# Kernel tuning notes

Measured on AMD Instinct MI355X. Metric: run time of the kernel, lower is better.

Reference implementation:

```python
import jax, jax.numpy as jnp
import numpy as np
import math

B, S, D = 4, 4096, 512

def setup_inputs() -> dict:
    key = jax.random.key(0)
    k_tok, k1, k2, k3 = jax.random.split(key, 4)
    scale = 1.0 / math.sqrt(D)
    return {
        "token": jax.random.normal(k_tok, (B, S, D), dtype=jnp.float32),
        "W1": jax.random.normal(k1, (D, D), dtype=jnp.float32) * scale,
        "W2": jax.random.normal(k2, (D, D), dtype=jnp.float32) * scale,
        "W3": jax.random.normal(k3, (D, D), dtype=jnp.float32) * scale,
    }

def reference(token, W1, W2, W3):
    # nn.Linear(dim, dim, bias=False): y = x @ W.T; W stored as [out, in]
    q = jnp.einsum('bsd,ed->bse', token, W1)  # t1(token)
    k = jnp.einsum('bsd,ed->bse', token, W2)  # t2(token)
    v = jnp.einsum('bsd,ed->bse', token, W3)  # t3(token)
    logits = jnp.einsum('bse,bte->bst', q, k) / jnp.sqrt(jnp.float32(token.shape[-1]))
    scores = jax.nn.softmax(logits, axis=-1)  # full [B,S,S] materialized, as in source
    return jnp.einsum('bst,bte->bse', scores, v)
```

## Files before the change

kernel.cpp:

```cpp
#include <hip/hip_runtime.h>
#include <stdint.h>


#define BDIM 4
#define SDIM 4096
#define DDIM 512
#define MROWS (BDIM * SDIM)
#define XB_ELEMS ((size_t)MROWS * DDIM)
#define W_ELEMS ((size_t)DDIM * DDIM)

typedef short short8_t __attribute__((ext_vector_type(8)));
typedef short short4_t __attribute__((ext_vector_type(4)));
typedef float float4_t __attribute__((ext_vector_type(4)));

typedef __attribute__((address_space(1))) void gvoid_t;
typedef __attribute__((address_space(3))) void lvoid_t;

__device__ __forceinline__ short f2bf(float f) {
    union { float f; uint32_t u; } v; v.f = f;
    uint32_t r = v.u + 0x7FFFu + ((v.u >> 16) & 1u);
    return (short)(r >> 16);
}
__device__ __forceinline__ float bf2f(short s) {
    union { uint32_t u; float f; } v; v.u = ((uint32_t)(uint16_t)s) << 16;
    return v.f;
}

__global__ void detect_kernel(const uint32_t* __restrict__ tok, int* __restrict__ flag) {
    __shared__ int red[256];
    const int tid = threadIdx.x;
    int c = 0;
    for (int i = tid; i < 4096; i += 256) {
        uint32_t e = (tok[i] >> 7) & 0xFFu;
        c += (e >= 105u && e <= 135u) ? 1 : 0;
    }
    red[tid] = c;
    __syncthreads();
    for (int s = 128; s > 0; s >>= 1) {
        if (tid < s) red[tid] += red[tid + s];
        __syncthreads();
    }
    if (tid == 0) *flag = (red[0] > 2048) ? 1 : 0;
}

__global__ void convert_kernel(const void* __restrict__ X, const void* __restrict__ W1,
                               const void* __restrict__ W2, const void* __restrict__ W3,
                               short* __restrict__ dst, const int* __restrict__ flagp,
                               float* __restrict__ RS)
{
    const int bid = blockIdx.x;
    if (bid < 64) RS[bid * 256 + threadIdx.x] = 0.f;
    const int bf16in = *flagp;
    if (bf16in) return;
    const size_t i4 = ((size_t)bid * 256 + threadIdx.x) * 4;
    const void* src; size_t off;
    if (i4 < XB_ELEMS) { src = X; off = i4; }
    else {
        const size_t j = i4 - XB_ELEMS;
        const int g = (int)(j / W_ELEMS);
        src = (g == 0) ? W1 : (g == 1) ? W2 : W3;
        off = j - (size_t)g * W_ELEMS;
    }
    float4 v = *(const float4*)((const float*)src + off);
    short4_t s = { f2bf(v.x), f2bf(v.y), f2bf(v.z), f2bf(v.w) };
    *(short4_t*)(dst + i4) = s;
}

__device__ __forceinline__ void gemm_core(
    const short* __restrict__ A, int lda,
    const short* __restrict__ B, int ldb,
    int m0, int n0, int kIters,
    short* As, short* Bs, float4_t acc[4][4])
{
    const int tid = threadIdx.x;
    const int w = tid >> 6, lane = tid & 63, quad = lane >> 4, l16 = lane & 15;
    const int wm = w >> 1, wn = w & 1;
    const int srow = lane >> 3;
    const int scol = 8 * ((lane & 7) ^ srow);
    const int rsw = l16 & 7;

    for (int kk = 0; kk < kIters; ++kk) {
        const int k0 = 64 * kk;
        __syncthreads();
#pragma unroll
        for (int c = 0; c < 4; ++c) {
            const int rb = 8 * (4 * c + w);
            const short* g = A + (size_t)(m0 + rb + srow) * lda + k0 + scol;
            __builtin_amdgcn_global_load_lds((const gvoid_t*)g,
                (lvoid_t*)(As + rb * 64), 16, 0, 0);
        }
#pragma unroll
        for (int c = 0; c < 4; ++c) {
            const int rb = 8 * (4 * c + w);
            const short* g = B + (size_t)(n0 + rb + srow) * ldb + k0 + scol;
            __builtin_amdgcn_global_load_lds((const gvoid_t*)g,
                (lvoid_t*)(Bs + rb * 64), 16, 0, 0);
        }
        __syncthreads();

#pragma unroll
        for (int k2 = 0; k2 < 2; ++k2) {
            short8_t af[4], bfr[4];
#pragma unroll
            for (int mt = 0; mt < 4; ++mt)
                af[mt] = *(const short8_t*)&As[(64 * wm + 16 * mt + l16) * 64
                                               + 8 * ((quad + 4 * k2) ^ rsw)];
#pragma unroll
            for (int nt = 0; nt < 4; ++nt)
                bfr[nt] = *(const short8_t*)&Bs[(64 * wn + 16 * nt + l16) * 64
                                                + 8 * ((quad + 4 * k2) ^ rsw)];
#pragma unroll
            for (int mt = 0; mt < 4; ++mt)
#pragma unroll
                for (int nt = 0; nt < 4; ++nt)
                    acc[mt][nt] = __builtin_amdgcn_mfma_f32_16x16x32_bf16(af[mt], bfr[nt], acc[mt][nt], 0, 0, 0);
        }
    }
}

__global__ void proj_fast(const short* __restrict__ XbWb,
                          const void* __restrict__ tokRaw, const void* __restrict__ W1r,
                          const void* __restrict__ W2r, const void* __restrict__ W3r,
                          const int* __restrict__ flagp, short* __restrict__ QKV)
{
    __shared__ __align__(16) short As[128 * 64];
    __shared__ __align__(16) short Bs[128 * 64];

    const int bf16in = *flagp;
    const short* Xb = bf16in ? (const short*)tokRaw : XbWb;
    const short* Wb[3] = {
        bf16in ? (const short*)W1r : XbWb + XB_ELEMS,
        bf16in ? (const short*)W2r : XbWb + XB_ELEMS + W_ELEMS,
        bf16in ? (const short*)W3r : XbWb + XB_ELEMS + 2 * W_ELEMS };

    const int bid = blockIdx.x;
    const int g = bid >> 9;
    const int r = bid & 511;

    const short* Ap; const short* Bp; short* Op;
    int m0, n0, ldo;
    if (g == 2) {
        Ap = Wb[2]; Bp = Xb;
        Op = QKV + 2 * (size_t)MROWS * DDIM;
        m0 = 128 * (r & 3); n0 = 128 * (r >> 2); ldo = MROWS;
    } else {
        Ap = Xb; Bp = Wb[g];
        Op = QKV + (size_t)g * MROWS * DDIM;
        m0 = 128 * (r >> 2); n0 = 128 * (r & 3); ldo = DDIM;
    }

    const float4_t z4 = {0.f, 0.f, 0.f, 0.f};
    float4_t acc[4][4];
#pragma unroll
    for (int i = 0; i < 4; ++i)
#pragma unroll
        for (int j = 0; j < 4; ++j) acc[i][j] = z4;

    gemm_core(Ap, DDIM, Bp, DDIM, m0, n0, 8, As, Bs, acc);

    const int tid = threadIdx.x;
    const int w = tid >> 6, lane = tid & 63, quad = lane >> 4, l16 = lane & 15;
    const int wm = w >> 1, wn = w & 1;
#pragma unroll
    for (int mt = 0; mt < 4; ++mt)
#pragma unroll
        for (int nt = 0; nt < 4; ++nt)
#pragma unroll
            for (int rr = 0; rr < 4; ++rr) {
                const int m = m0 + 64 * wm + 16 * mt + 4 * quad + rr;
                const int n = n0 + 64 * wn + 16 * nt + l16;
                Op[(size_t)m * ldo + n] = f2bf(acc[mt][nt][rr]);
            }
}

__global__ void qkt_kernel(const short* __restrict__ QKV, short* __restrict__ P,
                           float* __restrict__ RS, int bbase)
{
    __shared__ __align__(16) short As[128 * 64];
    __shared__ __align__(16) short Bs[128 * 64];

    const int bid = blockIdx.x;
    const int bb = bid >> 10;
    const int r = bid & 1023;
    const int b = bbase + bb;
    const int m0 = 128 * (r >> 5);
    const int n0 = 128 * (r & 31);

    const short* Qb = QKV + (size_t)b * SDIM * DDIM;
    const short* Kb = QKV + (size_t)MROWS * DDIM + (size_t)b * SDIM * DDIM;

    const float4_t z4 = {0.f, 0.f, 0.f, 0.f};
    float4_t acc[4][4];
#pragma unroll
    for (int i = 0; i < 4; ++i)
#pragma unroll
        for (int j = 0; j < 4; ++j) acc[i][j] = z4;

    gemm_core(Qb, DDIM, Kb, DDIM, m0, n0, 8, As, Bs, acc);

    const int tid = threadIdx.x;
    const int w = tid >> 6, lane = tid & 63, quad = lane >> 4, l16 = lane & 15;
    const int wm = w >> 1, wn = w & 1;
    const float kSc = 1.44269504088896341f * 0.04419417382415922f;
    short* Pb = P + (size_t)bb * SDIM * SDIM;
#pragma unroll
    for (int mt = 0; mt < 4; ++mt)
#pragma unroll
        for (int rr = 0; rr < 4; ++rr) {
            const int q = m0 + 64 * wm + 16 * mt + 4 * quad + rr;
            float sum = 0.f;
#pragma unroll
            for (int nt = 0; nt < 4; ++nt) {
                const float p = exp2f(acc[mt][nt][rr] * kSc);
                const short pb = f2bf(p);
                sum += bf2f(pb);
                Pb[(size_t)q * SDIM + n0 + 64 * wn + 16 * nt + l16] = pb;
            }
            sum += __shfl_xor(sum, 1); sum += __shfl_xor(sum, 2);
            sum += __shfl_xor(sum, 4); sum += __shfl_xor(sum, 8);
            if (l16 == 0) atomicAdd(&RS[(size_t)b * SDIM + q], sum);
        }
}

__global__ void pv_kernel(const short* __restrict__ P, const short* __restrict__ QKV,
                          const float* __restrict__ RS, void* __restrict__ out,
                          const int* __restrict__ flagp, int bbase)
{
    __shared__ __align__(16) short As[128 * 64];
    __shared__ __align__(16) short Bs[128 * 64];

    const int bf16out = *flagp;
    const int cpx = (int)(gridDim.x >> 3);
    const int bid = (int)blockIdx.x;
    const int l = (bid & 7) * cpx + (bid >> 3);
    const int bb = l >> 7;
    const int r = l & 127;
    const int b = bbase + bb;
    const int m0 = 128 * (r >> 2);
    const int n0 = 128 * (r & 3);

    const short* Pb = P + (size_t)bb * SDIM * SDIM;
    const short* Vt = QKV + 2 * (size_t)MROWS * DDIM + (size_t)b * SDIM;

    const float4_t z4 = {0.f, 0.f, 0.f, 0.f};
    float4_t acc[4][4];
#pragma unroll
    for (int i = 0; i < 4; ++i)
#pragma unroll
        for (int j = 0; j < 4; ++j) acc[i][j] = z4;

    gemm_core(Pb, SDIM, Vt, MROWS, m0, n0, 64, As, Bs, acc);

    const int tid = threadIdx.x;
    const int w = tid >> 6, lane = tid & 63, quad = lane >> 4, l16 = lane & 15;
    const int wm = w >> 1, wn = w & 1;
#pragma unroll
    for (int mt = 0; mt < 4; ++mt)
#pragma unroll
        for (int rr = 0; rr < 4; ++rr) {
            const size_t grow = (size_t)b * SDIM + m0 + 64 * wm + 16 * mt + 4 * quad + rr;
            const float inv = 1.0f / RS[grow];
#pragma unroll
            for (int nt = 0; nt < 4; ++nt) {
                const int n = n0 + 64 * wn + 16 * nt + l16;
                const float o = acc[mt][nt][rr] * inv;
                if (bf16out) ((short*)out)[grow * DDIM + n] = f2bf(o);
                else         ((float*)out)[grow * DDIM + n] = o;
            }
        }
}

__global__ void proj_mfma_legacy(const void* __restrict__ X, const void* __restrict__ W1,
                          const void* __restrict__ W2, const void* __restrict__ W3,
                          short* __restrict__ QKV, const int* __restrict__ flagp)
{
    __shared__ __align__(16) short As[128][40];
    __shared__ __align__(16) short Bs[128][40];

    const int bf16in = *flagp;
    const int bid = blockIdx.x;
    const int g = bid >> 9;
    const int r = bid & 511;

    const void* Ap; const void* Bp; short* Op;
    int m0, n0, ldo;
    if (g == 2) {
        Ap = W3; Bp = X; Op = QKV + 2 * (size_t)MROWS * DDIM;
        m0 = 128 * (r & 3); n0 = 128 * (r >> 2); ldo = MROWS;
    } else {
        Ap = X; Bp = (g == 0) ? W1 : W2; Op = QKV + (size_t)g * MROWS * DDIM;
        m0 = 128 * (r >> 2); n0 = 128 * (r & 3); ldo = DDIM;
    }

    const float* Af = (const float*)Ap;  const float* Bf = (const float*)Bp;
    const short* Ah = (const short*)Ap;  const short* Bh = (const short*)Bp;

    const int tid = threadIdx.x;
    const int w = tid >> 6, lane = tid & 63, quad = lane >> 4, l16 = lane & 15;
    const int wm = w >> 1, wn = w & 1;
    const int rgrp = tid >> 3, cg = tid & 7;

    const float4_t z4 = {0.f, 0.f, 0.f, 0.f};
    float4_t acc[4][4];
#pragma unroll
    for (int i = 0; i < 4; ++i)
#pragma unroll
        for (int j = 0; j < 4; ++j) acc[i][j] = z4;

    for (int kk = 0; kk < 16; ++kk) {
        const int k0 = 32 * kk;
        __syncthreads();
        if (bf16in) {
#pragma unroll
            for (int i = 0; i < 4; ++i) {
                const int row = rgrp + 32 * i;
                *(short4_t*)&As[row][4 * cg] =
                    *(const short4_t*)(Ah + (size_t)(m0 + row) * DDIM + k0 + 4 * cg);
                *(short4_t*)&Bs[row][4 * cg] =
                    *(const short4_t*)(Bh + (size_t)(n0 + row) * DDIM + k0 + 4 * cg);
            }
        } else {
#pragma unroll
            for (int i = 0; i < 4; ++i) {
                const int row = rgrp + 32 * i;
                float4 va = *(const float4*)(Af + (size_t)(m0 + row) * DDIM + k0 + 4 * cg);
                short4_t sa = { f2bf(va.x), f2bf(va.y), f2bf(va.z), f2bf(va.w) };
                *(short4_t*)&As[row][4 * cg] = sa;
                float4 vb = *(const float4*)(Bf + (size_t)(n0 + row) * DDIM + k0 + 4 * cg);
                short4_t sb = { f2bf(vb.x), f2bf(vb.y), f2bf(vb.z), f2bf(vb.w) };
                *(short4_t*)&Bs[row][4 * cg] = sb;
            }
        }
        __syncthreads();

        short8_t af[4], bfr[4];
#pragma unroll
        for (int mt = 0; mt < 4; ++mt)
            af[mt] = *(const short8_t*)&As[64 * wm + 16 * mt + l16][8 * quad];
#pragma unroll
        for (int nt = 0; nt < 4; ++nt)
            bfr[nt] = *(const short8_t*)&Bs[64 * wn + 16 * nt + l16][8 * quad];
#pragma unroll
        for (int mt = 0; mt < 4; ++mt)
#pragma unroll
            for (int nt = 0; nt < 4; ++nt)
                acc[mt][nt] = __builtin_amdgcn_mfma_f32_16x16x32_bf16(af[mt], bfr[nt], acc[mt][nt], 0, 0, 0);
    }

#pragma unroll
    for (int mt = 0; mt < 4; ++mt)
#pragma unroll
        for (int nt = 0; nt < 4; ++nt)
#pragma unroll
            for (int rr = 0; rr < 4; ++rr) {
                const int m = m0 + 64 * wm + 16 * mt + 4 * quad + rr;
                const int n = n0 + 64 * wn + 16 * nt + l16;
                Op[(size_t)m * ldo + n] = f2bf(acc[mt][nt][rr]);
            }
}

__global__ void attn_mfma(const short* __restrict__ QKV, void* __restrict__ out,
                          const int* __restrict__ flagp)
{
    __shared__ __align__(16) short Ks[32][520];
    __shared__ __align__(16) short Ps[32][72];
    __shared__ float rowsum[2][32];

    const int bf16out = *flagp;
    const short* Qb = QKV;
    const short* Kb = QKV + (size_t)MROWS * DDIM;
    const short* Vt = QKV + 2 * (size_t)MROWS * DDIM;

    const int b = blockIdx.x >> 7;
    const int q0 = (blockIdx.x & 127) * 32;
    const int tid = threadIdx.x;
    const int w = tid >> 6, lane = tid & 63, quad = lane >> 4, l16 = lane & 15;
    const int strip = w >> 1, half = w & 1;

    short8_t qf[16];
    {
        const short* qrow = Qb + (size_t)(b * SDIM + q0 + 16 * strip + l16) * DDIM + 8 * quad;
#pragma unroll
        for (int kc = 0; kc < 16; ++kc)
            qf[kc] = *(const short8_t*)(qrow + 32 * kc);
    }

    const float4_t z4 = {0.f, 0.f, 0.f, 0.f};
    float4_t o[2][8];
#pragma unroll
    for (int mt = 0; mt < 2; ++mt)
#pragma unroll
        for (int nt = 0; nt < 8; ++nt) o[mt][nt] = z4;
    float rs[4] = {0.f, 0.f, 0.f, 0.f};

    const float kSc = 1.44269504088896341f * 0.04419417382415922f;

    for (int kt = 0; kt < 128; ++kt) {
        const int kv0 = 32 * kt;
        __syncthreads();
#pragma unroll
        for (int r = 0; r < 8; ++r) {
            const int kv = 8 * w + r;
            short8_t t = *(const short8_t*)(Kb + (size_t)(b * SDIM + kv0 + kv) * DDIM + 8 * lane);
            *(short8_t*)&Ks[kv][8 * lane] = t;
        }
        __syncthreads();

        float4_t sacc = z4;
#pragma unroll
        for (int kc = 0; kc < 16; ++kc) {
            short8_t kf = *(const short8_t*)&Ks[16 * half + l16][32 * kc + 8 * quad];
            sacc = __builtin_amdgcn_mfma_f32_16x16x32_bf16(qf[kc], kf, sacc, 0, 0, 0);
        }

#pragma unroll
        for (int r = 0; r < 4; ++r) {
            const float p = exp2f(sacc[r] * kSc);
            const short pb = f2bf(p);
            rs[r] += bf2f(pb);
            Ps[16 * strip + 4 * quad + r][16 * half + l16] = pb;
        }
        __syncthreads();

        short8_t pa0 = *(const short8_t*)&Ps[l16][8 * quad];
        short8_t pa1 = *(const short8_t*)&Ps[16 + l16][8 * quad];
#pragma unroll
        for (int nt = 0; nt < 8; ++nt) {
            const short* vp = Vt + (size_t)(128 * w + 16 * nt + l16) * MROWS
                            + (b * SDIM + kv0 + 8 * quad);
            short8_t vb = *(const short8_t*)vp;
            o[0][nt] = __builtin_amdgcn_mfma_f32_16x16x32_bf16(pa0, vb, o[0][nt], 0, 0, 0);
            o[1][nt] = __builtin_amdgcn_mfma_f32_16x16x32_bf16(pa1, vb, o[1][nt], 0, 0, 0);
        }
    }

#pragma unroll
    for (int r = 0; r < 4; ++r) {
        float v = rs[r];
        v += __shfl_xor(v, 1); v += __shfl_xor(v, 2);
        v += __shfl_xor(v, 4); v += __shfl_xor(v, 8);
        rs[r] = v;
    }
    if (l16 == 0) {
#pragma unroll
        for (int r = 0; r < 4; ++r)
            rowsum[half][16 * strip + 4 * quad + r] = rs[r];
    }
    __syncthreads();

#pragma unroll
    for (int mt = 0; mt < 2; ++mt)
#pragma unroll
        for (int r = 0; r < 4; ++r) {
            const int q = 16 * mt + 4 * quad + r;
            const float inv = 1.0f / (rowsum[0][q] + rowsum[1][q]);
            const size_t base = (size_t)(b * SDIM + q0 + q) * DDIM + 128 * w + l16;
            if (bf16out) {
                short* orow = (short*)out + base;
#pragma unroll
                for (int nt = 0; nt < 8; ++nt)
                    orow[16 * nt] = f2bf(o[mt][nt][r] * inv);
            } else {
                float* orow = (float*)out + base;
#pragma unroll
                for (int nt = 0; nt < 8; ++nt)
                    orow[16 * nt] = o[mt][nt][r] * inv;
            }
        }
}

__global__ void zero_out_kernel(short* __restrict__ out, int n) {
    int i = blockIdx.x * 256 + threadIdx.x;
    if (i < n) out[i] = 0;
}

extern "C" void kernel_launch(void* const* d_in, const int* in_sizes, int n_in,
                              void* d_out, int out_size, void* d_ws, size_t ws_size,
                              hipStream_t stream) {
    const void* token = d_in[0];
    const void* Wp[3] = { d_in[1], d_in[2], d_in[3] };
    {
        int wi = 0;
        const void* tk = nullptr; const void* ws3[3] = {nullptr, nullptr, nullptr};
        bool ok = true;
        for (int i = 0; i < n_in && i < 4; ++i) {
            if (in_sizes[i] == BDIM * SDIM * DDIM) { if (tk) ok = false; tk = d_in[i]; }
            else if (in_sizes[i] == DDIM * DDIM) { if (wi < 3) ws3[wi++] = d_in[i]; else ok = false; }
            else ok = false;
        }
        if (ok && tk && wi == 3) { token = tk; Wp[0] = ws3[0]; Wp[1] = ws3[1]; Wp[2] = ws3[2]; }
    }

    const size_t qkvBytes = 3 * (size_t)MROWS * DDIM * sizeof(short);
    const size_t need_base = qkvBytes + 256;
    if (ws_size < need_base) {
        zero_out_kernel<<<(out_size + 255) / 256, 256, 0, stream>>>((short*)d_out, out_size);
        return;
    }

    short* QKV = (short*)d_ws;
    int* flag = (int*)((char*)d_ws + qkvBytes);
    short* P = (short*)((char*)d_ws + need_base);
    const size_t pElems1 = (size_t)SDIM * SDIM;

    int nb = 0;
    for (int cand = 4; cand >= 1; cand >>= 1) {
        const size_t need = need_base + (size_t)cand * pElems1 * sizeof(short)
                          + (size_t)MROWS * sizeof(float);
        if (ws_size >= need) { nb = cand; break; }
    }

    detect_kernel<<<1, 256, 0, stream>>>((const uint32_t*)token, flag);

    if (nb == 0) {
        proj_mfma_legacy<<<dim3(1536), 256, 0, stream>>>(token, Wp[0], Wp[1], Wp[2], QKV, flag);
        attn_mfma<<<dim3(512), 256, 0, stream>>>(QKV, d_out, flag);
        return;
    }

    short* XbWb = P;
    float* RS = (float*)(P + (size_t)nb * pElems1);
    const size_t cvt4 = (XB_ELEMS + 3 * W_ELEMS) / 4;
    convert_kernel<<<dim3((unsigned)(cvt4 / 256)), 256, 0, stream>>>(
        token, Wp[0], Wp[1], Wp[2], XbWb, flag, RS);
    proj_fast<<<dim3(1536), 256, 0, stream>>>(XbWb, token, Wp[0], Wp[1], Wp[2], flag, QKV);

    for (int p = 0; p < BDIM / nb; ++p) {
        const int bbase = p * nb;
        qkt_kernel<<<dim3(nb * 1024), 256, 0, stream>>>(QKV, P, RS, bbase);
        pv_kernel<<<dim3(nb * 128), 256, 0, stream>>>(P, QKV, RS, d_out, flag, bbase);
    }
}
```

Baseline: 305.9 us.

## Split PV GEMM along key dimension with atomic accumulation and finish kernel

Replaces the single PV kernel with a split-K version that divides the 4096-long key dimension into two halves. This doubles the block count, so more of the GPU's compute units are occupied. Partial results are atomically added into an fp32 buffer, which the convert kernel now zeroes. A new finish kernel then normalizes by the row sums and writes the output. The cost is extra fp32 atomic traffic, an added 32MB buffer round trip, and one more launch.

```diff
diff --git a/kernel.cpp b/kernel.cpp
--- a/kernel.cpp
+++ b/kernel.cpp
@@ -46,13 +46,18 @@
 __global__ void convert_kernel(const void* __restrict__ X, const void* __restrict__ W1,
                                const void* __restrict__ W2, const void* __restrict__ W3,
                                short* __restrict__ dst, const int* __restrict__ flagp,
-                               float* __restrict__ RS)
+                               float* __restrict__ RS, float* __restrict__ Oacc, int ozn)
 {
     const int bid = blockIdx.x;
-    if (bid < 64) RS[bid * 256 + threadIdx.x] = 0.f;
+    const int tid = threadIdx.x;
+    if (bid < 64) RS[bid * 256 + tid] = 0.f;
+    if (bid < ozn) {
+        const float4_t z4 = {0.f, 0.f, 0.f, 0.f};
+        *(float4_t*)(Oacc + ((size_t)bid * 256 + tid) * 4) = z4;
+    }
     const int bf16in = *flagp;
     if (bf16in) return;
-    const size_t i4 = ((size_t)bid * 256 + threadIdx.x) * 4;
+    const size_t i4 = ((size_t)bid * 256 + tid) * 4;
     const void* src; size_t off;
     if (i4 < XB_ELEMS) { src = X; off = i4; }
     else {
@@ -220,6 +225,67 @@
             sum += __shfl_xor(sum, 4); sum += __shfl_xor(sum, 8);
             if (l16 == 0) atomicAdd(&RS[(size_t)b * SDIM + q], sum);
         }
+}
+
+__global__ void pv_split_kernel(const short* __restrict__ P, const short* __restrict__ QKV,
+                                float* __restrict__ Oacc, int bbase)
+{
+    __shared__ __align__(16) short As[128 * 64];
+    __shared__ __align__(16) short Bs[128 * 64];
+
+    const int cpx = (int)(gridDim.x >> 3);
+    const int bid = (int)blockIdx.x;
+    const int l = (bid & 7) * cpx + (bid >> 3);
+    const int bb = l >> 8;
+    const int r = l & 255;
+    const int b = bbase + bb;
+    const int n0 = 128 * (r & 3);
+    const int ks = (r >> 2) & 1;
+    const int m0 = 128 * (r >> 3);
+
+    const short* Pb = P + (size_t)bb * SDIM * SDIM + ks * 2048;
+    const short* Vt = QKV + 2 * (size_t)MROWS * DDIM + (size_t)b * SDIM + ks * 2048;
+
+    const float4_t z4 = {0.f, 0.f, 0.f, 0.f};
+    float4_t acc[4][4];
+#pragma unroll
+    for (int i = 0; i < 4; ++i)
+#pragma unroll
+        for (int j = 0; j < 4; ++j) acc[i][j] = z4;
+
+    gemm_core(Pb, SDIM, Vt, MROWS, m0, n0, 32, As, Bs, acc);
+
+    const int tid = threadIdx.x;
+    const int w = tid >> 6, lane = tid & 63, quad = lane >> 4, l16 = lane & 15;
+    const int wm = w >> 1, wn = w & 1;
+#pragma unroll
+    for (int mt = 0; mt < 4; ++mt)
+#pragma unroll
+        for (int rr = 0; rr < 4; ++rr) {
+            const size_t grow = (size_t)b * SDIM + m0 + 64 * wm + 16 * mt + 4 * quad + rr;
+#pragma unroll
+            for (int nt = 0; nt < 4; ++nt) {
+                const int n = n0 + 64 * wn + 16 * nt + l16;
+                atomicAdd(&Oacc[grow * DDIM + n], acc[mt][nt][rr]);
+            }
+        }
+}
+
+__global__ void pv_finish_kernel(const float* __restrict__ Oacc, const float* __restrict__ RS,
+                                 void* __restrict__ out, const int* __restrict__ flagp)
+{
+    const int bf16out = *flagp;
+    const size_t i4 = ((size_t)blockIdx.x * 256 + threadIdx.x) * 4;
+    const size_t row = i4 >> 9;
+    const float inv = 1.0f / RS[row];
+    const float4_t v = *(const float4_t*)(Oacc + i4);
+    if (bf16out) {
+        short4_t s = { f2bf(v[0] * inv), f2bf(v[1] * inv), f2bf(v[2] * inv), f2bf(v[3] * inv) };
+        *(short4_t*)((short*)out + i4) = s;
+    } else {
+        float4_t o = { v[0] * inv, v[1] * inv, v[2] * inv, v[3] * inv };
+        *(float4_t*)((float*)out + i4) = o;
+    }
 }
 
 __global__ void pv_kernel(const short* __restrict__ P, const short* __restrict__ QKV,
@@ -520,14 +586,26 @@
 
     short* XbWb = P;
     float* RS = (float*)(P + (size_t)nb * pElems1);
+    float* Oacc = RS + MROWS;
+    const size_t needSplit = need_base + (size_t)nb * pElems1 * sizeof(short)
+                           + (size_t)MROWS * sizeof(float)
+                           + (size_t)MROWS * DDIM * sizeof(float);
+    const bool useSplit = (nb == 4) && (ws_size >= needSplit);
+
     const size_t cvt4 = (XB_ELEMS + 3 * W_ELEMS) / 4;
     convert_kernel<<<dim3((unsigned)(cvt4 / 256)), 256, 0, stream>>>(
-        token, Wp[0], Wp[1], Wp[2], XbWb, flag, RS);
+        token, Wp[0], Wp[1], Wp[2], XbWb, flag, RS,
+        useSplit ? Oacc : RS , useSplit ? 8192 : 0);
     proj_fast<<<dim3(1536), 256, 0, stream>>>(XbWb, token, Wp[0], Wp[1], Wp[2], flag, QKV);
 
     for (int p = 0; p < BDIM / nb; ++p) {
         const int bbase = p * nb;
         qkt_kernel<<<dim3(nb * 1024), 256, 0, stream>>>(QKV, P, RS, bbase);
-        pv_kernel<<<dim3(nb * 128), 256, 0, stream>>>(P, QKV, RS, d_out, flag, bbase);
-    }
-}
+        if (useSplit)
+            pv_split_kernel<<<dim3(nb * 256), 256, 0, stream>>>(P, QKV, Oacc, bbase);
+        else
+            pv_kernel<<<dim3(nb * 128), 256, 0, stream>>>(P, QKV, RS, d_out, flag, bbase);
+    }
+    if (useSplit)
+        pv_finish_kernel<<<dim3(8192), 256, 0, stream>>>(Oacc, RS, d_out, flag);
+}
```

After: 334.7 us. 1.09x slower.
